# Performance work log

Measured on AMD Instinct MI355X. Metric: run time of the kernel, lower is better.

## Reference

```python
import jax, jax.numpy as jnp
import numpy as np
from jax import lax

NEG = jnp.float32(-1e30)  # log(0) stand-in, safe for logsumexp in fp32


def _ctc_loss(logits, labels, blank=0):
    """Per-example CTC loss (negative log-likelihood), logits [B,T,V],
    labels [B,L] dense with 0 = padding. Full input_length = T."""
    B, T, V = logits.shape
    L = labels.shape[1]
    S = 2 * L + 1  # extended label length: blank interleaved

    logp = jax.nn.log_softmax(logits, axis=-1)  # [B,T,V]
    label_length = jnp.sum((labels != 0).astype(jnp.int32), axis=1)  # [B]

    # extended sequence: ext[2k] = blank, ext[2k+1] = labels[k]
    ext = jnp.full((B, S), blank, dtype=jnp.int32).at[:, 1::2].set(labels.astype(jnp.int32))

    # gather per-timestep log-prob of each extended symbol -> [B,T,S]
    lp_ext = jnp.take_along_axis(logp, jnp.broadcast_to(ext[:, None, :], (B, T, S)), axis=2)

    # skip (s-2 -> s) allowed only for non-blank symbols different from s-2
    same_as_prev2 = jnp.concatenate(
        [jnp.ones((B, 2), dtype=bool), ext[:, 2:] == ext[:, :-2]], axis=1)
    skip_mask = (ext != blank) & (~same_as_prev2)  # [B,S]

    # alpha_0: start at s=0 (blank) or s=1 (first label)
    alpha0 = jnp.full((B, S), NEG, dtype=logp.dtype)
    alpha0 = alpha0.at[:, 0].set(lp_ext[:, 0, 0])
    alpha0 = alpha0.at[:, 1].set(lp_ext[:, 0, 1])

    lp_seq = jnp.transpose(lp_ext, (1, 0, 2))  # [T,B,S]

    def step(alpha, lp_t):
        a1 = jnp.concatenate([jnp.full((B, 1), NEG, alpha.dtype), alpha[:, :-1]], axis=1)
        a2 = jnp.concatenate([jnp.full((B, 2), NEG, alpha.dtype), alpha[:, :-2]], axis=1)
        a2 = jnp.where(skip_mask, a2, NEG)
        new = jax.nn.logsumexp(jnp.stack([alpha, a1, a2]), axis=0) + lp_t
        return new, None

    alpha_T, _ = lax.scan(step, alpha0, lp_seq[1:])

    # terminal states: last blank (2*len) and last label (2*len-1)
    end_blank = (2 * label_length)[:, None]
    end_label = jnp.maximum(2 * label_length - 1, 0)[:, None]
    v1 = jnp.take_along_axis(alpha_T, end_blank, axis=1)[:, 0]
    v2 = jnp.take_along_axis(alpha_T, end_label, axis=1)[:, 0]
    return -jnp.logaddexp(v1, v2)  # [B]


def setup_inputs() -> dict:
    key = jax.random.key(0)
    k1, k2, k3 = jax.random.split(key, 3)
    B, T, V, L = 64, 1000, 512, 256
    y_pred = jax.random.normal(k1, (B, T, V), dtype=jnp.float32)
    labels = jax.random.randint(k2, (B, L), 1, V)  # tokens in [1, V), 0 reserved for pad/blank
    lengths = jax.random.randint(k3, (B,), L // 2, L + 1)
    y_true = jnp.where(jnp.arange(L)[None, :] < lengths[:, None], labels, 0).astype(jnp.int64)
    return {"y_pred": y_pred, "y_true": y_true}


def reference(y_pred, y_true):
    # CTCLossLayer computes tf.nn.ctc_loss per example (blank_index=0,
    # logit_length = T, label_length = #nonzero labels). We return the
    # per-example loss vector, the quantity the layer reduces via add_loss.
    return _ctc_loss(y_pred, y_true, blank=0)
```

## Files before the change

kernel.cpp:

```cpp
#include <hip/hip_runtime.h>
#include <math.h>

#define BB 64
#define TT 1000
#define VV 512
#define LL 256
#define NEG2 (-1.0e30f)
#define KK 3
#define LOG2E 1.4426950408889634f
#define LN2   0.6931471805599453f

#if __has_builtin(__builtin_amdgcn_exp2f)
#define EXP2(x) __builtin_amdgcn_exp2f(x)
#else
#define EXP2(x) __expf((x) * LN2)
#endif
#if __has_builtin(__builtin_amdgcn_logf)
#define LOG2(x) __builtin_amdgcn_logf(x)
#else
#define LOG2(x) (__logf(x) * LOG2E)
#endif

__global__ __launch_bounds__(256) void ctc_lse_kernel(
    const float* __restrict__ logits, float* __restrict__ lse) {
  int wave = threadIdx.x >> 6;
  int lane = threadIdx.x & 63;
  int row  = blockIdx.x * 4 + wave;
  const float4* p = (const float4*)(logits + (size_t)row * VV);
  float4 a = p[lane];
  float4 c = p[lane + 64];
  float m = fmaxf(fmaxf(fmaxf(a.x, a.y), fmaxf(a.z, a.w)),
                  fmaxf(fmaxf(c.x, c.y), fmaxf(c.z, c.w)));
  #pragma unroll
  for (int off = 32; off; off >>= 1) m = fmaxf(m, __shfl_xor(m, off, 64));
  float s = __expf(a.x - m) + __expf(a.y - m) + __expf(a.z - m) + __expf(a.w - m)
          + __expf(c.x - m) + __expf(c.y - m) + __expf(c.z - m) + __expf(c.w - m);
  #pragma unroll
  for (int off = 32; off; off >>= 1) s += __shfl_xor(s, off, 64);
  if (lane == 0) lse[row] = m + __logf(s);
}

__global__ __launch_bounds__(256) void ctc_dp_kernel(
    const float* __restrict__ logits, const int* __restrict__ labels,
    const float* __restrict__ lse, float* __restrict__ out) {
  __shared__ __align__(16) float ABUF[2][524];
  __shared__ float LPo[2][KK][LL];
  __shared__ float red[4];
  __shared__ int   nzcnt[4];

  const int b   = blockIdx.x;
  const int tid = threadIdx.x;
  const int* lab = labels + b * LL;

  {
    bool nz = (lab[tid] != 0);
    unsigned long long mask = __ballot(nz);
    if ((tid & 63) == 0) nzcnt[tid >> 6] = __popcll(mask);
  }

  unsigned skipm = 0;
  #pragma unroll
  for (int j = 0; j < 6; j += 2) {
    int u = 2 * tid + 1 - j;
    if (u >= 3) {
      int k = u >> 1;
      int v = lab[k], vp = lab[k - 1];
      if (v != 0 && v != vp) skipm |= (1u << j);
    }
  }

  const int mysym = lab[tid];
  const float* gmy = logits + (size_t)b * TT * VV + mysym;
  const float* gbl = logits + (size_t)b * TT * VV;

  if (tid < 8) { ABUF[0][tid] = NEG2; ABUF[1][tid] = NEG2; }
  if (tid == 0) {
    ABUF[0][8 + 0] = gbl[0] * LOG2E;
    ABUF[0][8 + 1] = gmy[0] * LOG2E;
  } else {
    ABUF[0][8 + 2 * tid]     = NEG2;
    ABUF[0][8 + 2 * tid + 1] = NEG2;
  }
  float a512 = NEG2;

  #pragma unroll
  for (int i = 0; i < KK; ++i)
    LPo[0][i][tid] = gmy[(size_t)(1 + i) * VV] * LOG2E;
  float blk0 = gbl[(size_t)1 * VV] * LOG2E;
  float blk1 = gbl[(size_t)2 * VV] * LOG2E;
  float blk2 = gbl[(size_t)3 * VV] * LOG2E;

  float sg[3][KK], bg[3][KK];
  #pragma unroll
  for (int s = 0; s < 3; ++s) {
    #pragma unroll
    for (int i = 0; i < KK; ++i) {
      int t = 4 + 3 * s + i;
      sg[s][i] = gmy[(size_t)t * VV];
      bg[s][i] = gbl[(size_t)t * VV];
    }
  }

  int p = 0, n = 0;

#define SUPERSTEP(S)                                                          \
  {                                                                           \
    asm volatile("s_waitcnt lgkmcnt(0)" ::: "memory");                        \
    __builtin_amdgcn_s_barrier();                                             \
    __builtin_amdgcn_sched_barrier(0);                                        \
              \
    float cur[8];                                                             \
    {                                                                         \
      const float2* h2 = (const float2*)&ABUF[p][2 * tid + 2];                \
      float2 r0 = h2[0], r1 = h2[1], r2 = h2[2], r3 = h2[3];                  \
      cur[7] = r0.x; cur[6] = r0.y; cur[5] = r1.x; cur[4] = r1.y;             \
      cur[3] = r2.x; cur[2] = r2.y; cur[1] = r3.x; cur[0] = r3.y;             \
    }                                                                         \
            \
    _Pragma("unroll")                                                         \
    for (int i = 0; i < KK; ++i) LPo[p ^ 1][i][tid] = sg[S][i] * LOG2E;       \
    float nb0 = bg[S][0] * LOG2E, nb1 = bg[S][1] * LOG2E,                     \
          nb2 = bg[S][2] * LOG2E;                                             \
       \
    _Pragma("unroll")                                                         \
    for (int i = 0; i < KK; ++i) {                                            \
      int t = 3 * n + 13 + i; t = (t > TT - 1) ? (TT - 1) : t;                \
      sg[S][i] = gmy[(size_t)t * VV];                                         \
      bg[S][i] = gbl[(size_t)t * VV];                                         \
    }                                                                         \
    _Pragma("unroll")                                                         \
    for (int i = 1; i <= KK; ++i) {                                           \
      float p511 = cur[0];                                                    \
      float lbi = (i == 1) ? blk0 : (i == 2) ? blk1 : blk2;                   \
      _Pragma("unroll")                                                       \
      for (int j = 0; j < 2 * (KK - i) + 2; ++j) {                            \
        float aa = cur[j], bb = cur[j + 1];                                   \
        if ((j & 1) == 0) {                  \
          float cc = (skipm & (1u << j)) ? cur[j + 2] : NEG2;                 \
          float mm = fmaxf(fmaxf(aa, bb), cc);                                \
          float ss = EXP2(aa - mm) + EXP2(bb - mm) + EXP2(cc - mm);           \
          int mi = tid - (j >> 1); mi = mi < 0 ? 0 : mi;                      \
          cur[j] = mm + LOG2(ss) + LPo[p][i - 1][mi];                         \
        } else {                                       \
          float mm = fmaxf(aa, bb);                                           \
          float ss = EXP2(aa - mm) + EXP2(bb - mm);                           \
          cur[j] = mm + LOG2(ss) + lbi;                                       \
        }                                                                     \
      }                                                                       \
      if (tid == 255) {     \
        float mm = fmaxf(a512, p511);                                         \
        a512 = mm + LOG2(EXP2(a512 - mm) + EXP2(p511 - mm)) + lbi;            \
      }                                                                       \
    }                                                                         \
    ((float2*)&ABUF[p ^ 1][8 + 2 * tid])[0] = make_float2(cur[1], cur[0]);    \
    blk0 = nb0; blk1 = nb1; blk2 = nb2;                                       \
    p ^= 1; ++n;                                                              \
  }

  for (int it = 0; it < 111; ++it) {
    SUPERSTEP(0)
    SUPERSTEP(1)
    SUPERSTEP(2)
  }
#undef SUPERSTEP

  if (tid == 255) ABUF[p][8 + 512] = a512;

  const float* lrow = lse + b * TT;
  float ls = lrow[tid] + lrow[tid + 256] + lrow[tid + 512];
  if (tid < TT - 768) ls += lrow[tid + 768];
  #pragma unroll
  for (int off = 32; off; off >>= 1) ls += __shfl_xor(ls, off, 64);
  if ((tid & 63) == 0) red[tid >> 6] = ls;
  __syncthreads();

  if (tid == 0) {
    int len = nzcnt[0] + nzcnt[1] + nzcnt[2] + nzcnt[3];
    int eb = 2 * len;
    int el = eb - 1; if (el < 0) el = 0;
    float v1 = ABUF[p][8 + eb];
    float v2 = ABUF[p][8 + el];
    float mm = fmaxf(v1, v2);
    float l2 = mm + LOG2(EXP2(v1 - mm) + EXP2(v2 - mm));
    out[b] = (red[0] + red[1] + red[2] + red[3]) - l2 * LN2;
  }
}

extern "C" void kernel_launch(void* const* d_in, const int* in_sizes, int n_in,
                              void* d_out, int out_size, void* d_ws, size_t ws_size,
                              hipStream_t stream) {
  const float* logits = (const float*)d_in[0];
  const int*   labels = (const int*)d_in[1];
  float* out = (float*)d_out;
  float* lse = (float*)d_ws;

  ctc_lse_kernel<<<(BB * TT) / 4, 256, 0, stream>>>(logits, lse);
  ctc_dp_kernel<<<BB, 256, 0, stream>>>(logits, labels, lse, out);
}
```

Measured before the change: 431.3 us.

## Compute CTC alpha superstep in scaled linear domain with pre-exponentiated emissions

Replaces the per-cell log-sum-exp recurrence with a linear-domain computation. Each thread rescales its seven input alphas by a local max, exponentiates once, and runs three timesteps of multiply-add on emission probabilities that are exponentiated in advance. The result is converted back to log2 only at the end, which removes most exp2/log2 calls from the serial critical path. The global prefetch ring shrinks from three slots to two, with the loop restructured to match. Over three steps without renormalisation this risks underflow, since emission probabilities near 1/V can push small values to zero and they are then clamped to NEG2.

```diff
diff --git a/kernel.cpp b/kernel.cpp
--- a/kernel.cpp
+++ b/kernel.cpp
@@ -44,7 +44,7 @@
     const float* __restrict__ logits, const int* __restrict__ labels,
     const float* __restrict__ lse, float* __restrict__ out) {
   __shared__ __align__(16) float ABUF[2][524];
-  __shared__ float LPo[2][KK][LL];
+  __shared__ float LPE[2][KK][LL];
   __shared__ float red[4];
   __shared__ int   nzcnt[4];
 
@@ -68,6 +68,8 @@
       if (v != 0 && v != vp) skipm |= (1u << j);
     }
   }
+  const int mi1 = (tid >= 1) ? tid - 1 : 0;
+  const int mi2 = (tid >= 2) ? tid - 2 : 0;
 
   const int mysym = lab[tid];
   const float* gmy = logits + (size_t)b * TT * VV + mysym;
@@ -85,14 +87,14 @@
 
   #pragma unroll
   for (int i = 0; i < KK; ++i)
-    LPo[0][i][tid] = gmy[(size_t)(1 + i) * VV] * LOG2E;
-  float blk0 = gbl[(size_t)1 * VV] * LOG2E;
-  float blk1 = gbl[(size_t)2 * VV] * LOG2E;
-  float blk2 = gbl[(size_t)3 * VV] * LOG2E;
-
-  float sg[3][KK], bg[3][KK];
-  #pragma unroll
-  for (int s = 0; s < 3; ++s) {
+    LPE[0][i][tid] = EXP2(gmy[(size_t)(1 + i) * VV] * LOG2E);
+  float be0 = EXP2(gbl[(size_t)1 * VV] * LOG2E);
+  float be1 = EXP2(gbl[(size_t)2 * VV] * LOG2E);
+  float be2 = EXP2(gbl[(size_t)3 * VV] * LOG2E);
+
+  float sg[2][KK], bg[2][KK];
+  #pragma unroll
+  for (int s = 0; s < 2; ++s) {
     #pragma unroll
     for (int i = 0; i < KK; ++i) {
       int t = 4 + 3 * s + i;
@@ -106,62 +108,76 @@
 #define SUPERSTEP(S)                                                          \
   {                                                                           \
     asm volatile("s_waitcnt lgkmcnt(0)" ::: "memory");                        \
+    __builtin_amdgcn_sched_barrier(0);                                        \
     __builtin_amdgcn_s_barrier();                                             \
     __builtin_amdgcn_sched_barrier(0);                                        \
-              \
-    float cur[8];                                                             \
-    {                                                                         \
-      const float2* h2 = (const float2*)&ABUF[p][2 * tid + 2];                \
-      float2 r0 = h2[0], r1 = h2[1], r2 = h2[2], r3 = h2[3];                  \
-      cur[7] = r0.x; cur[6] = r0.y; cur[5] = r1.x; cur[4] = r1.y;             \
-      cur[3] = r2.x; cur[2] = r2.y; cur[1] = r3.x; cur[0] = r3.y;             \
-    }                                                                         \
-            \
-    _Pragma("unroll")                                                         \
-    for (int i = 0; i < KK; ++i) LPo[p ^ 1][i][tid] = sg[S][i] * LOG2E;       \
-    float nb0 = bg[S][0] * LOG2E, nb1 = bg[S][1] * LOG2E,                     \
-          nb2 = bg[S][2] * LOG2E;                                             \
+                      \
+    const float2* h2 = (const float2*)&ABUF[p][2 * tid + 2];                  \
+    float2 r0 = h2[0], r1 = h2[1], r2 = h2[2], r3 = h2[3];                    \
+    float c6 = r0.y, c5 = r1.x, c4 = r1.y, c3 = r2.x,                         \
+          c2 = r2.y, c1 = r3.x, c0 = r3.y;                                    \
+                      \
+    const float* LP0 = &LPE[p][0][0];                                         \
+    float e00 = LP0[tid], e01 = LP0[mi1], e02 = LP0[mi2];                     \
+    float e10 = LP0[LL + tid], e11 = LP0[LL + mi1];                           \
+    float e20 = LP0[2 * LL + tid];                                            \
        \
+    float* LPn = &LPE[p ^ 1][0][0];                                           \
+    LPn[tid]          = EXP2(sg[S][0] * LOG2E);                               \
+    LPn[LL + tid]     = EXP2(sg[S][1] * LOG2E);                               \
+    LPn[2 * LL + tid] = EXP2(sg[S][2] * LOG2E);                               \
+    float nb0 = EXP2(bg[S][0] * LOG2E);                                       \
+    float nb1 = EXP2(bg[S][1] * LOG2E);                                       \
+    float nb2 = EXP2(bg[S][2] * LOG2E);                                       \
+          \
     _Pragma("unroll")                                                         \
     for (int i = 0; i < KK; ++i) {                                            \
-      int t = 3 * n + 13 + i; t = (t > TT - 1) ? (TT - 1) : t;                \
+      int t = 3 * n + 10 + i; t = (t > TT - 1) ? (TT - 1) : t;                \
       sg[S][i] = gmy[(size_t)t * VV];                                         \
       bg[S][i] = gbl[(size_t)t * VV];                                         \
     }                                                                         \
-    _Pragma("unroll")                                                         \
-    for (int i = 1; i <= KK; ++i) {                                           \
-      float p511 = cur[0];                                                    \
-      float lbi = (i == 1) ? blk0 : (i == 2) ? blk1 : blk2;                   \
-      _Pragma("unroll")                                                       \
-      for (int j = 0; j < 2 * (KK - i) + 2; ++j) {                            \
-        float aa = cur[j], bb = cur[j + 1];                                   \
-        if ((j & 1) == 0) {                  \
-          float cc = (skipm & (1u << j)) ? cur[j + 2] : NEG2;                 \
-          float mm = fmaxf(fmaxf(aa, bb), cc);                                \
-          float ss = EXP2(aa - mm) + EXP2(bb - mm) + EXP2(cc - mm);           \
-          int mi = tid - (j >> 1); mi = mi < 0 ? 0 : mi;                      \
-          cur[j] = mm + LOG2(ss) + LPo[p][i - 1][mi];                         \
-        } else {                                       \
-          float mm = fmaxf(aa, bb);                                           \
-          float ss = EXP2(aa - mm) + EXP2(bb - mm);                           \
-          cur[j] = mm + LOG2(ss) + lbi;                                       \
-        }                                                                     \
-      }                                                                       \
-      if (tid == 255) {     \
-        float mm = fmaxf(a512, p511);                                         \
-        a512 = mm + LOG2(EXP2(a512 - mm) + EXP2(p511 - mm)) + lbi;            \
-      }                                                                       \
-    }                                                                         \
-    ((float2*)&ABUF[p ^ 1][8 + 2 * tid])[0] = make_float2(cur[1], cur[0]);    \
-    blk0 = nb0; blk1 = nb1; blk2 = nb2;                                       \
+                         \
+    float mloc = fmaxf(fmaxf(fmaxf(c0, c1), fmaxf(c2, c3)),                   \
+                       fmaxf(fmaxf(c4, c5), c6));                             \
+    float p0 = EXP2(c0 - mloc), p1 = EXP2(c1 - mloc), p2 = EXP2(c2 - mloc);   \
+    float p3 = EXP2(c3 - mloc), p4 = EXP2(c4 - mloc), p5 = EXP2(c5 - mloc);   \
+    float p6 = EXP2(c6 - mloc);                                               \
+    float pe512 = EXP2(a512 - mloc);                                          \
+                                                     \
+    float q511 = p0;                                                          \
+    float s0 = (p0 + p1 + ((skipm & 1u)  ? p2 : 0.f)) * e00;                  \
+    float s1 = (p1 + p2) * be0;                                               \
+    float s2 = (p2 + p3 + ((skipm & 4u)  ? p4 : 0.f)) * e01;                  \
+    float s3 = (p3 + p4) * be0;                                               \
+    float s4 = (p4 + p5 + ((skipm & 16u) ? p6 : 0.f)) * e02;                  \
+    float s5 = (p5 + p6) * be0;                                               \
+    pe512 = (pe512 + q511) * be0;                                             \
+                                                     \
+    q511 = s0;                                                                \
+    float u0 = (s0 + s1 + ((skipm & 1u) ? s2 : 0.f)) * e10;                   \
+    float u1 = (s1 + s2) * be1;                                               \
+    float u2 = (s2 + s3 + ((skipm & 4u) ? s4 : 0.f)) * e11;                   \
+    float u3 = (s3 + s4) * be1;                                               \
+    pe512 = (pe512 + q511) * be1;                                             \
+                                                     \
+    q511 = u0;                                                                \
+    float f0 = (u0 + u1 + ((skipm & 1u) ? u2 : 0.f)) * e20;                   \
+    float f1 = (u1 + u2) * be2;                                               \
+    pe512 = (pe512 + q511) * be2;                                             \
+                   \
+    float w1 = fmaxf(mloc + LOG2(f0), NEG2);                \
+    float w0 = fmaxf(mloc + LOG2(f1), NEG2);                \
+    a512 = fmaxf(mloc + LOG2(pe512), NEG2);    \
+    ((float2*)&ABUF[p ^ 1][8 + 2 * tid])[0] = make_float2(w0, w1);            \
+    be0 = nb0; be1 = nb1; be2 = nb2;                                          \
     p ^= 1; ++n;                                                              \
   }
 
-  for (int it = 0; it < 111; ++it) {
+  for (int it = 0; it < 166; ++it) {
     SUPERSTEP(0)
     SUPERSTEP(1)
-    SUPERSTEP(2)
-  }
+  }
+  SUPERSTEP(0)
 #undef SUPERSTEP
 
   if (tid == 255) ABUF[p][8 + 512] = a512;
```

New measurement: 389.1 us. -9.8%, faster.
